# Optimization experiments

Measured on AMD Instinct MI355X. Metric: run time of the kernel, lower is better.

The kernel has to match this reference:

```python
import jax, jax.numpy as jnp
import numpy as np


def _conv3x3(x, w, stride=1):
    # x: [N, C_in, H, W], w: [C_out, C_in, 3, 3] (ternary {-1,0,1}), padding=1, no bias
    return jax.lax.conv_general_dilated(
        x, w,
        window_strides=(stride, stride),
        padding=((1, 1), (1, 1)),
        dimension_numbers=("NCHW", "OIHW", "NCHW"),
    )


def _bn(x, gamma, beta, mean, var, eps=1e-5):
    # inference-mode BatchNorm2d over channel dim
    inv = gamma * jax.lax.rsqrt(var + eps)
    return x * inv[None, :, None, None] + (beta - mean * inv)[None, :, None, None]


def setup_inputs() -> dict:
    key = jax.random.key(0)
    ks = jax.random.split(key, 8)
    N, C, H, W = 64, 256, 32, 32
    x = jax.random.normal(ks[0], (N, C, H, W), dtype=jnp.float32)
    # Ternary conv weights in {-1, 0, +1} (scale_and_shift=False => raw ternary values)
    w1 = jax.random.randint(ks[1], (C, C, 3, 3), -1, 2).astype(jnp.float32)
    w2 = jax.random.randint(ks[2], (C, C, 3, 3), -1, 2).astype(jnp.float32)
    # BatchNorm affine params and running stats
    g1 = jax.random.normal(ks[3], (C,), dtype=jnp.float32) * 0.1 + 1.0
    b1 = jax.random.normal(ks[4], (C,), dtype=jnp.float32) * 0.1
    g2 = jax.random.normal(ks[5], (C,), dtype=jnp.float32) * 0.1 + 1.0
    b2 = jax.random.normal(ks[6], (C,), dtype=jnp.float32) * 0.1
    rm1 = jnp.zeros((C,), dtype=jnp.float32)
    rv1 = jnp.ones((C,), dtype=jnp.float32)
    rm2 = jnp.zeros((C,), dtype=jnp.float32)
    rv2 = jnp.ones((C,), dtype=jnp.float32)
    return {"x": x, "w1": w1, "g1": g1, "b1": b1, "rm1": rm1, "rv1": rv1,
            "w2": w2, "g2": g2, "b2": b2, "rm2": rm2, "rv2": rv2}


def reference(x, w1, g1, b1, rm1, rv1, w2, g2, b2, rm2, rv2):
    # BasicBlock forward: stride=1, downsample=None -> identity skip
    h = _conv3x3(x, w1, stride=1)
    h = _bn(h, g1, b1, rm1, rv1)
    h = jax.nn.relu(h)
    h = _conv3x3(h, w2, stride=1)
    h = _bn(h, g2, b2, rm2, rv2)
    return jax.nn.relu(x + h)
```

## Files before the change

### kernel.cpp

```cpp
#include <hip/hip_runtime.h>

typedef unsigned short u16;
typedef unsigned int u32;
typedef __attribute__((ext_vector_type(8))) short bf16x8;
typedef __attribute__((ext_vector_type(4))) float f32x4;

__device__ __forceinline__ u16 f2bf(float f) {
    u32 u = __float_as_uint(f);
    u += 0x7fffu + ((u >> 16) & 1u);
    return (u16)(u >> 16);
}

__device__ __forceinline__ void llds16(void* l, const void* g) {
    __builtin_amdgcn_global_load_lds(
        (const __attribute__((address_space(1))) u32*)g,
        (__attribute__((address_space(3))) u32*)l, 16, 0, 0);
}

__global__ void prep(const float* __restrict__ x, u16* __restrict__ xt,
                     const float* __restrict__ w1, const float* __restrict__ w2,
                     u16* __restrict__ W1t, u16* __restrict__ W2t,
                     const float* __restrict__ g1, const float* __restrict__ b1,
                     const float* __restrict__ rm1, const float* __restrict__ rv1,
                     const float* __restrict__ g2, const float* __restrict__ b2,
                     const float* __restrict__ rm2, const float* __restrict__ rv2,
                     float* __restrict__ sc, u32* __restrict__ zp) {
    int t = threadIdx.x;
    int b = blockIdx.x;
    if (b < 16384) {
        __shared__ float xl[32 * 33];
        int n = b >> 8, rem = b & 255;
        int h = rem >> 3, c0 = (rem & 7) << 5;
        int cl = t >> 5, w = t & 31;
#pragma unroll
        for (int i = 0; i < 4; ++i) {
            int c = c0 + i * 8 + cl;
            xl[(i * 8 + cl) * 33 + w] = x[(n * 256 + c) * 1024 + h * 32 + w];
        }
        __syncthreads();
        int wo = t >> 3, k = t & 7;
        ushort4 o;
        o.x = f2bf(xl[(k * 4 + 0) * 33 + wo]);
        o.y = f2bf(xl[(k * 4 + 1) * 33 + wo]);
        o.z = f2bf(xl[(k * 4 + 2) * 33 + wo]);
        o.w = f2bf(xl[(k * 4 + 3) * 33 + wo]);
        *(ushort4*)&xt[((n * 32 + h) * 32 + wo) * 256 + c0 + k * 4] = o;
    } else {
        int bb = b - 16384;
        int idx = (bb & 255) * 256 + t;
        const float* src = (bb >> 8) ? w2 : w1;
        u16* dst = (bb >> 8) ? W2t : W1t;
        const float* s = src + idx * 9;
        int co = idx >> 8, ci = idx & 255;
#pragma unroll
        for (int p = 0; p < 9; ++p)
            dst[p * 65536 + co * 256 + ci] = f2bf(s[p]);
        if (bb == 0) {
            float s1 = g1[t] * rsqrtf(rv1[t] + 1e-5f);
            sc[t]       = s1;
            sc[256 + t] = b1[t] - rm1[t] * s1;
            float s2 = g2[t] * rsqrtf(rv2[t] + 1e-5f);
            sc[512 + t] = s2;
            sc[768 + t] = b2[t] - rm2[t] * s2;
            zp[t] = 0u;
            zp[t + 256] = 0u;
        }
    }
}

__global__ __launch_bounds__(256, 2) void conv_mfma(
    const u16* __restrict__ Xt,
    const u16* __restrict__ Wt,
    const float* __restrict__ sv,
    const float* __restrict__ tv,
    const float* __restrict__ skip,
    u16* __restrict__ ybf,
    float* __restrict__ yf,
    const u16* __restrict__ zp, int stage)
{
    __shared__ alignas(16) u16 ldsA[9 * 4 * 64 * 8];
    __shared__ alignas(16) u16 ldsB[22 * 64 * 8];

    int t = threadIdx.x;
    int wv = t >> 6, lane = t & 63;
    int q = lane >> 4, n16 = lane & 15;

    int bid = blockIdx.x;
    int co_t = (bid >> 3) & 3;
    int sp   = ((bid >> 5) << 3) | (bid & 7);
    int h_t  = sp & 3, nb = sp >> 2;
    int co0 = co_t << 6, h0 = h_t << 3;

    const u16* aSrc[9];
#pragma unroll
    for (int i = 0; i < 9; ++i) {
        int g = wv * 9 + i;
        int p = g >> 2, mt = g & 3;
        aSrc[i] = Wt + (p << 16) + ((co0 + (mt << 4) + n16) << 8) + (q << 3);
    }
    const u16* bSrc[6];
#pragma unroll
    for (int j = 0; j < 6; ++j) {
        int g2 = wv * 6 + j;
        if (g2 < 22) {
            int s = g2 * 64 + lane;
            int hi = s / 136, rem = s - hi * 136;
            int wp = rem >> 2, qq = rem & 3;
            int hin = h0 - 1 + hi;
            bool v = (wp >= 1) && (wp <= 32) && (hin >= 0) && (hin < 32);
            bSrc[j] = v ? (Xt + (((nb << 5) + hin) * 32 + (wp - 1)) * 256 + (qq << 3))
                        : (zp + lane * 8);
        } else {
            bSrc[j] = zp + lane * 8;
        }
    }

    f32x4 acc[4][4] = {};

    for (int kc = 0; kc < 256; kc += 32) {
#pragma unroll
        for (int i = 0; i < 9; ++i)
            llds16(&ldsA[(wv * 9 + i) << 9], aSrc[i] + kc);
#pragma unroll
        for (int j = 0; j < 6; ++j) {
            int g2 = wv * 6 + j;
            if (g2 < 22) llds16(&ldsB[g2 << 9], bSrc[j] + kc);
        }
        asm volatile("s_waitcnt vmcnt(0)" ::: "memory");
        __syncthreads();

#pragma unroll
        for (int kw = 0; kw < 3; ++kw) {
            bf16x8 bFr[4][2];
#pragma unroll
            for (int r = 0; r < 4; ++r)
#pragma unroll
                for (int half = 0; half < 2; ++half) {
                    int hi = (wv << 1) + r;
                    int wp = (half << 4) + n16 + kw;
                    bFr[r][half] = *(const bf16x8*)
                        &ldsB[(hi * 136 + (wp << 2) + q) << 3];
                }
#pragma unroll
            for (int kh = 0; kh < 3; ++kh) {
                int p = kh * 3 + kw;
                bf16x8 aF[4];
#pragma unroll
                for (int mt = 0; mt < 4; ++mt)
                    aF[mt] = *(const bf16x8*)&ldsA[((p << 8) + (mt << 6) + lane) << 3];
#pragma unroll
                for (int mt = 0; mt < 4; ++mt)
#pragma unroll
                    for (int nt = 0; nt < 4; ++nt)
                        acc[mt][nt] = __builtin_amdgcn_mfma_f32_16x16x32_bf16(
                            aF[mt], bFr[(nt >> 1) + kh][nt & 1], acc[mt][nt], 0, 0, 0);
            }
        }
        __syncthreads();
    }

    if (stage == 1) {
#pragma unroll
        for (int mt = 0; mt < 4; ++mt) {
            int cb = co0 + (mt << 4) + (q << 2);
            f32x4 ss = *(const f32x4*)&sv[cb];
            f32x4 tt = *(const f32x4*)&tv[cb];
#pragma unroll
            for (int nt = 0; nt < 4; ++nt) {
                int h = h0 + (wv << 1) + (nt >> 1), w = ((nt & 1) << 4) + n16;
                ushort4 o;
                o.x = f2bf(fmaxf(acc[mt][nt][0] * ss[0] + tt[0], 0.f));
                o.y = f2bf(fmaxf(acc[mt][nt][1] * ss[1] + tt[1], 0.f));
                o.z = f2bf(fmaxf(acc[mt][nt][2] * ss[2] + tt[2], 0.f));
                o.w = f2bf(fmaxf(acc[mt][nt][3] * ss[3] + tt[3], 0.f));
                *(ushort4*)&ybf[(((nb << 5) + h) * 32 + w) * 256 + cb] = o;
            }
        }
    } else {
#pragma unroll
        for (int mt = 0; mt < 4; ++mt) {
            int cb = co0 + (mt << 4) + (q << 2);
            f32x4 ss = *(const f32x4*)&sv[cb];
            f32x4 tt = *(const f32x4*)&tv[cb];
#pragma unroll
            for (int nt = 0; nt < 4; ++nt) {
                int h = h0 + (wv << 1) + (nt >> 1), w = ((nt & 1) << 4) + n16;
#pragma unroll
                for (int j = 0; j < 4; ++j) {
                    int idx = (((nb << 8) + cb + j) << 10) + (h << 5) + w;
                    yf[idx] = fmaxf(acc[mt][nt][j] * ss[j] + tt[j] + skip[idx], 0.f);
                }
            }
        }
    }
}

extern "C" void kernel_launch(void* const* d_in, const int* in_sizes, int n_in,
                              void* d_out, int out_size, void* d_ws, size_t ws_size,
                              hipStream_t stream) {
    const float* x   = (const float*)d_in[0];
    const float* w1  = (const float*)d_in[1];
    const float* g1  = (const float*)d_in[2];
    const float* b1  = (const float*)d_in[3];
    const float* rm1 = (const float*)d_in[4];
    const float* rv1 = (const float*)d_in[5];
    const float* w2  = (const float*)d_in[6];
    const float* g2  = (const float*)d_in[7];
    const float* b2  = (const float*)d_in[8];
    const float* rm2 = (const float*)d_in[9];
    const float* rv2 = (const float*)d_in[10];

    char* ws = (char*)d_ws;
    u16*  XT  = (u16*)(ws);
    u16*  H1  = (u16*)(ws + 33554432);
    u16*  W1t = (u16*)(ws + 67108864);
    u16*  W2t = (u16*)(ws + 68288512);
    float* sc = (float*)(ws + 69468160);
    u32*  zpg = (u32*)(ws + 69472256);
    if (ws_size < 69474304) return;

    prep<<<16896, 256, 0, stream>>>(x, XT, w1, w2, W1t, W2t,
                                    g1, b1, rm1, rv1, g2, b2, rm2, rv2,
                                    sc, zpg);

    conv_mfma<<<1024, 256, 0, stream>>>(XT, W1t, sc, sc + 256, nullptr,
                                        H1, nullptr, (const u16*)zpg, 1);
    conv_mfma<<<1024, 256, 0, stream>>>(H1, W2t, sc + 512, sc + 768, x,
                                        nullptr, (float*)d_out, (const u16*)zpg, 2);
}
```

Baseline: 262.0 us.

## Double-buffer LDS loads and double the spatial tile per conv block

The conv kernel now uses two LDS buffers so global-to-LDS loads for the next K chunk overlap with MFMA work on the current one, waiting on vmcnt instead of draining all loads. Each block now covers 16 output rows instead of 8, doubling accumulators per wave and halving the grid to 512 blocks. This improves reuse of the weight tile per input halo. It adds wave priority hints and scheduling barriers. The cost is more registers and LDS (launch bounds drop to one block per SIMD set), lower occupancy, and fewer blocks than before to spread over the CUs.

```diff
diff --git a/kernel.cpp b/kernel.cpp
--- a/kernel.cpp
+++ b/kernel.cpp
@@ -68,7 +68,7 @@
     }
 }
 
-__global__ __launch_bounds__(256, 2) void conv_mfma(
+__global__ __launch_bounds__(256, 1) void conv_mfma(
     const u16* __restrict__ Xt,
     const u16* __restrict__ Wt,
     const float* __restrict__ sv,
@@ -78,8 +78,8 @@
     float* __restrict__ yf,
     const u16* __restrict__ zp, int stage)
 {
-    __shared__ alignas(16) u16 ldsA[9 * 4 * 64 * 8];
-    __shared__ alignas(16) u16 ldsB[22 * 64 * 8];
+    __shared__ alignas(16) u16 ldsA[2][9 * 4 * 64 * 8];
+    __shared__ alignas(16) u16 ldsB[2][40 * 64 * 8];
 
     int t = threadIdx.x;
     int wv = t >> 6, lane = t & 63;
@@ -88,8 +88,8 @@
     int bid = blockIdx.x;
     int co_t = (bid >> 3) & 3;
     int sp   = ((bid >> 5) << 3) | (bid & 7);
-    int h_t  = sp & 3, nb = sp >> 2;
-    int co0 = co_t << 6, h0 = h_t << 3;
+    int h_t  = sp & 1, nb = sp >> 1;
+    int co0 = co_t << 6, h0 = h_t << 4;
 
     const u16* aSrc[9];
 #pragma unroll
@@ -98,48 +98,59 @@
         int p = g >> 2, mt = g & 3;
         aSrc[i] = Wt + (p << 16) + ((co0 + (mt << 4) + n16) << 8) + (q << 3);
     }
-    const u16* bSrc[6];
-#pragma unroll
-    for (int j = 0; j < 6; ++j) {
-        int g2 = wv * 6 + j;
-        if (g2 < 22) {
-            int s = g2 * 64 + lane;
-            int hi = s / 136, rem = s - hi * 136;
-            int wp = rem >> 2, qq = rem & 3;
-            int hin = h0 - 1 + hi;
-            bool v = (wp >= 1) && (wp <= 32) && (hin >= 0) && (hin < 32);
-            bSrc[j] = v ? (Xt + (((nb << 5) + hin) * 32 + (wp - 1)) * 256 + (qq << 3))
-                        : (zp + lane * 8);
+    const u16* bSrc[10];
+#pragma unroll
+    for (int j = 0; j < 10; ++j) {
+        int g2 = wv * 10 + j;
+        int s = g2 * 64 + lane;
+        int hi = s / 136, rem = s - hi * 136;
+        int wp = rem >> 2, qq = rem & 3;
+        int hin = h0 - 1 + hi;
+        bool v = (wp >= 1) && (wp <= 32) && (hin >= 0) && (hin < 32);
+        bSrc[j] = v ? (Xt + (((nb << 5) + hin) * 32 + (wp - 1)) * 256 + (qq << 3))
+                    : (zp + lane * 8);
+    }
+
+    f32x4 acc[4][8] = {};
+
+#pragma unroll
+    for (int i = 0; i < 9; ++i)
+        llds16(&ldsA[0][(wv * 9 + i) << 9], aSrc[i]);
+#pragma unroll
+    for (int j = 0; j < 10; ++j)
+        llds16(&ldsB[0][(wv * 10 + j) << 9], bSrc[j]);
+
+    int c = 0;
+    for (int kt = 0; kt < 8; ++kt) {
+        if (kt < 7) {
+            int kc = (kt + 1) << 5;
+#pragma unroll
+            for (int i = 0; i < 9; ++i)
+                llds16(&ldsA[c ^ 1][(wv * 9 + i) << 9], aSrc[i] + kc);
+#pragma unroll
+            for (int j = 0; j < 10; ++j)
+                llds16(&ldsB[c ^ 1][(wv * 10 + j) << 9], bSrc[j] + kc);
+            asm volatile("s_waitcnt vmcnt(19)" ::: "memory");
         } else {
-            bSrc[j] = zp + lane * 8;
-        }
-    }
-
-    f32x4 acc[4][4] = {};
-
-    for (int kc = 0; kc < 256; kc += 32) {
-#pragma unroll
-        for (int i = 0; i < 9; ++i)
-            llds16(&ldsA[(wv * 9 + i) << 9], aSrc[i] + kc);
-#pragma unroll
-        for (int j = 0; j < 6; ++j) {
-            int g2 = wv * 6 + j;
-            if (g2 < 22) llds16(&ldsB[g2 << 9], bSrc[j] + kc);
-        }
-        asm volatile("s_waitcnt vmcnt(0)" ::: "memory");
-        __syncthreads();
-
+            asm volatile("s_waitcnt vmcnt(0)" ::: "memory");
+        }
+        __builtin_amdgcn_s_barrier();
+        __builtin_amdgcn_sched_barrier(0);
+
+        const u16* pA = ldsA[c];
+        const u16* pB = ldsB[c];
+        __builtin_amdgcn_s_setprio(1);
 #pragma unroll
         for (int kw = 0; kw < 3; ++kw) {
-            bf16x8 bFr[4][2];
-#pragma unroll
-            for (int r = 0; r < 4; ++r)
+            bf16x8 bFr[6][2];
+#pragma unroll
+            for (int r = 0; r < 6; ++r)
 #pragma unroll
                 for (int half = 0; half < 2; ++half) {
-                    int hi = (wv << 1) + r;
+                    int hi = (wv << 2) + r;
                     int wp = (half << 4) + n16 + kw;
                     bFr[r][half] = *(const bf16x8*)
-                        &ldsB[(hi * 136 + (wp << 2) + q) << 3];
+                        &pB[(hi * 136 + (wp << 2) + q) << 3];
                 }
 #pragma unroll
             for (int kh = 0; kh < 3; ++kh) {
@@ -147,16 +158,19 @@
                 bf16x8 aF[4];
 #pragma unroll
                 for (int mt = 0; mt < 4; ++mt)
-                    aF[mt] = *(const bf16x8*)&ldsA[((p << 8) + (mt << 6) + lane) << 3];
+                    aF[mt] = *(const bf16x8*)&pA[((p << 8) + (mt << 6) + lane) << 3];
 #pragma unroll
                 for (int mt = 0; mt < 4; ++mt)
 #pragma unroll
-                    for (int nt = 0; nt < 4; ++nt)
+                    for (int nt = 0; nt < 8; ++nt)
                         acc[mt][nt] = __builtin_amdgcn_mfma_f32_16x16x32_bf16(
                             aF[mt], bFr[(nt >> 1) + kh][nt & 1], acc[mt][nt], 0, 0, 0);
             }
         }
-        __syncthreads();
+        __builtin_amdgcn_s_setprio(0);
+        __builtin_amdgcn_sched_barrier(0);
+        __builtin_amdgcn_s_barrier();
+        c ^= 1;
     }
 
     if (stage == 1) {
@@ -166,8 +180,8 @@
             f32x4 ss = *(const f32x4*)&sv[cb];
             f32x4 tt = *(const f32x4*)&tv[cb];
 #pragma unroll
-            for (int nt = 0; nt < 4; ++nt) {
-                int h = h0 + (wv << 1) + (nt >> 1), w = ((nt & 1) << 4) + n16;
+            for (int nt = 0; nt < 8; ++nt) {
+                int h = h0 + (wv << 2) + (nt >> 1), w = ((nt & 1) << 4) + n16;
                 ushort4 o;
                 o.x = f2bf(fmaxf(acc[mt][nt][0] * ss[0] + tt[0], 0.f));
                 o.y = f2bf(fmaxf(acc[mt][nt][1] * ss[1] + tt[1], 0.f));
@@ -183,8 +197,8 @@
             f32x4 ss = *(const f32x4*)&sv[cb];
             f32x4 tt = *(const f32x4*)&tv[cb];
 #pragma unroll
-            for (int nt = 0; nt < 4; ++nt) {
-                int h = h0 + (wv << 1) + (nt >> 1), w = ((nt & 1) << 4) + n16;
+            for (int nt = 0; nt < 8; ++nt) {
+                int h = h0 + (wv << 2) + (nt >> 1), w = ((nt & 1) << 4) + n16;
 #pragma unroll
                 for (int j = 0; j < 4; ++j) {
                     int idx = (((nb << 8) + cb + j) << 10) + (h << 5) + w;
@@ -223,8 +237,8 @@
                                     g1, b1, rm1, rv1, g2, b2, rm2, rv2,
                                     sc, zpg);
 
-    conv_mfma<<<1024, 256, 0, stream>>>(XT, W1t, sc, sc + 256, nullptr,
-                                        H1, nullptr, (const u16*)zpg, 1);
-    conv_mfma<<<1024, 256, 0, stream>>>(H1, W2t, sc + 512, sc + 768, x,
-                                        nullptr, (float*)d_out, (const u16*)zpg, 2);
-}
+    conv_mfma<<<512, 256, 0, stream>>>(XT, W1t, sc, sc + 256, nullptr,
+                                       H1, nullptr, (const u16*)zpg, 1);
+    conv_mfma<<<512, 256, 0, stream>>>(H1, W2t, sc + 512, sc + 768, x,
+                                       nullptr, (float*)d_out, (const u16*)zpg, 2);
+}
```

New measurement: 306.7 us. 1.17x slower.

## Overlap next K-chunk global-to-LDS loads with last kw MFMA pass

Applied to the files above, without the earlier changes.

The K loop is restructured so the last kw slice's A and B fragments are preloaded into registers. After a barrier, the next K-chunk's global_load_lds transfers are issued, and the final 48 MFMAs then run from registers while those transfers are in flight. This hides part of the global load latency that the old load-wait-compute loop exposed. It also adds s_setprio around the MFMA blocks, at the cost of higher register pressure (12 extra A fragments plus 8 B fragments) under launch_bounds(256,2).

```diff
diff --git a/kernel.cpp b/kernel.cpp
--- a/kernel.cpp
+++ b/kernel.cpp
@@ -117,20 +117,21 @@
 
     f32x4 acc[4][4] = {};
 
-    for (int kc = 0; kc < 256; kc += 32) {
-#pragma unroll
-        for (int i = 0; i < 9; ++i)
-            llds16(&ldsA[(wv * 9 + i) << 9], aSrc[i] + kc);
-#pragma unroll
-        for (int j = 0; j < 6; ++j) {
-            int g2 = wv * 6 + j;
-            if (g2 < 22) llds16(&ldsB[g2 << 9], bSrc[j] + kc);
-        }
+#pragma unroll
+    for (int i = 0; i < 9; ++i)
+        llds16(&ldsA[(wv * 9 + i) << 9], aSrc[i]);
+#pragma unroll
+    for (int j = 0; j < 6; ++j) {
+        int g2 = wv * 6 + j;
+        if (g2 < 22) llds16(&ldsB[g2 << 9], bSrc[j]);
+    }
+
+    for (int kt = 0; kt < 8; ++kt) {
         asm volatile("s_waitcnt vmcnt(0)" ::: "memory");
-        __syncthreads();
-
-#pragma unroll
-        for (int kw = 0; kw < 3; ++kw) {
+        __builtin_amdgcn_s_barrier();
+
+#pragma unroll
+        for (int kw = 0; kw < 2; ++kw) {
             bf16x8 bFr[4][2];
 #pragma unroll
             for (int r = 0; r < 4; ++r)
@@ -141,6 +142,7 @@
                     bFr[r][half] = *(const bf16x8*)
                         &ldsB[(hi * 136 + (wp << 2) + q) << 3];
                 }
+            __builtin_amdgcn_s_setprio(1);
 #pragma unroll
             for (int kh = 0; kh < 3; ++kh) {
                 int p = kh * 3 + kw;
@@ -155,8 +157,54 @@
                         acc[mt][nt] = __builtin_amdgcn_mfma_f32_16x16x32_bf16(
                             aF[mt], bFr[(nt >> 1) + kh][nt & 1], acc[mt][nt], 0, 0, 0);
             }
-        }
-        __syncthreads();
+            __builtin_amdgcn_s_setprio(0);
+        }
+
+        bf16x8 bF2[4][2];
+        bf16x8 aF2[3][4];
+#pragma unroll
+        for (int r = 0; r < 4; ++r)
+#pragma unroll
+            for (int half = 0; half < 2; ++half) {
+                int hi = (wv << 1) + r;
+                int wp = (half << 4) + n16 + 2;
+                bF2[r][half] = *(const bf16x8*)
+                    &ldsB[(hi * 136 + (wp << 2) + q) << 3];
+            }
+#pragma unroll
+        for (int kh = 0; kh < 3; ++kh) {
+            int p = kh * 3 + 2;
+#pragma unroll
+            for (int mt = 0; mt < 4; ++mt)
+                aF2[kh][mt] = *(const bf16x8*)&ldsA[((p << 8) + (mt << 6) + lane) << 3];
+        }
+        asm volatile("s_waitcnt lgkmcnt(0)" ::: "memory");
+        __builtin_amdgcn_sched_barrier(0);
+        __builtin_amdgcn_s_barrier();
+
+        if (kt < 7) {
+            int kc = (kt + 1) << 5;
+#pragma unroll
+            for (int i = 0; i < 9; ++i)
+                llds16(&ldsA[(wv * 9 + i) << 9], aSrc[i] + kc);
+#pragma unroll
+            for (int j = 0; j < 6; ++j) {
+                int g2 = wv * 6 + j;
+                if (g2 < 22) llds16(&ldsB[g2 << 9], bSrc[j] + kc);
+            }
+        }
+        __builtin_amdgcn_sched_barrier(0);
+
+        __builtin_amdgcn_s_setprio(1);
+#pragma unroll
+        for (int kh = 0; kh < 3; ++kh)
+#pragma unroll
+            for (int mt = 0; mt < 4; ++mt)
+#pragma unroll
+                for (int nt = 0; nt < 4; ++nt)
+                    acc[mt][nt] = __builtin_amdgcn_mfma_f32_16x16x32_bf16(
+                        aF2[kh][mt], bF2[(nt >> 1) + kh][nt & 1], acc[mt][nt], 0, 0, 0);
+        __builtin_amdgcn_s_setprio(0);
     }
 
     if (stage == 1) {
```

After: 267.5 us. 2.1% more time.
